# Kernel tuning notes

Hardware: AMD Instinct MI355X
Metric: run time of the kernel (lower is better)

Reference implementation:

```python
import jax, jax.numpy as jnp
import numpy as np

EMB = 512
HEAD = 64
B, S = 4, 4096


def setup_inputs() -> dict:
    key = jax.random.key(0)
    kq, kk, kv, kwq, kwk, kwv = jax.random.split(key, 6)
    q = jax.random.normal(kq, (B, S, EMB), dtype=jnp.float32)
    k = jax.random.normal(kk, (B, S, EMB), dtype=jnp.float32)
    v = jax.random.normal(kv, (B, S, EMB), dtype=jnp.float32)
    # nn.Linear weights: [out_features, in_features], no bias
    sc = 1.0 / np.sqrt(EMB)
    Wq = jax.random.uniform(kwq, (HEAD, EMB), jnp.float32, -sc, sc)
    Wk = jax.random.uniform(kwk, (HEAD, EMB), jnp.float32, -sc, sc)
    Wv = jax.random.uniform(kwv, (HEAD, EMB), jnp.float32, -sc, sc)
    return {"q": q, "k": k, "v": v, "Wq": Wq, "Wk": Wk, "Wv": Wv}


def reference(q, k, v, Wq, Wk, Wv):
    scale = 1.0 / np.sqrt(HEAD).astype(np.float32)
    Q = jnp.einsum('bse,he->bsh', q, Wq)  # [B,S,HEAD]
    K = jnp.einsum('bse,he->bsh', k, Wk)
    V = jnp.einsum('bse,he->bsh', v, Wv)
    scores = jnp.einsum('bqh,bkh->bqk', Q, K) * scale  # [B,S,S]
    attn = jax.nn.softmax(scores, axis=-1)
    # dropout p=0.0 -> identity
    out = jnp.einsum('bqk,bkh->bqh', attn, V)  # [B,S,HEAD]
    return out
```

## Files before the change

### kernel.cpp

```cpp
#include <hip/hip_runtime.h>
#include <hip/hip_bf16.h>

#define EMB    512
#define HEAD   64
#define SEQ    4096
#define NB     4
#define NSPLIT 8
#define LDX    72

#define SL2E   0.18033688011112042f

typedef __bf16 bf16x8 __attribute__((ext_vector_type(8)));
typedef float  f32x4  __attribute__((ext_vector_type(4)));

__device__ inline ushort4 cvt4(float4 v) {
    __hip_bfloat16 a = __float2bfloat16(v.x), b = __float2bfloat16(v.y);
    __hip_bfloat16 c = __float2bfloat16(v.z), d = __float2bfloat16(v.w);
    ushort4 r;
    r.x = *(unsigned short*)&a; r.y = *(unsigned short*)&b;
    r.z = *(unsigned short*)&c; r.w = *(unsigned short*)&d;
    return r;
}

__global__ __launch_bounds__(256) void cvtw_kernel(
    const float* __restrict__ Wq, const float* __restrict__ Wk,
    const float* __restrict__ Wv, __hip_bfloat16* __restrict__ Wc)
{
    int idx   = blockIdx.x * 256 + threadIdx.x;
    int which = idx >> 13;
    int off   = (idx & 8191) * 4;
    const float* src = (which == 0) ? Wq : (which == 1) ? Wk : Wv;
    float s = (which == 0) ? SL2E : 1.0f;
    float4 v = *(const float4*)(src + off);
    v.x *= s; v.y *= s; v.z *= s; v.w *= s;
    *(ushort4*)(Wc + which * 64 * EMB + off) = cvt4(v);
}

__global__ __launch_bounds__(256) void proj_kernel(
    const float* __restrict__ q, const float* __restrict__ k, const float* __restrict__ v,
    const __hip_bfloat16* __restrict__ Wc,
    __hip_bfloat16* __restrict__ Qo, __hip_bfloat16* __restrict__ Ko,
    __hip_bfloat16* __restrict__ Vto)
{
    __shared__ __hip_bfloat16 Xs[32][LDX];

    const int which = blockIdx.y;
    const float* __restrict__ x = (which == 0) ? q : (which == 1) ? k : v;
    const __hip_bfloat16* __restrict__ W = Wc + which * 64 * EMB;

    const int tid  = threadIdx.x;
    const int wave = tid >> 6, lane = tid & 63;
    const int l16  = lane & 15, quad = lane >> 4;
    const int rs   = (wave & 1) * 16;
    const int ch   = wave >> 1;
    const int r0   = blockIdx.x * 32;
    const float* __restrict__ xb = x + (size_t)r0 * EMB;

    const int sr = tid >> 4;
    const int sc = (tid & 15) << 2;

    const f32x4 z = {0.f, 0.f, 0.f, 0.f};
    f32x4 acc[2] = {z, z};

    float4 xr[2];
    bf16x8 wf[4];

#define LOADX(dst, e0)                                                        \
    _Pragma("unroll")                                                         \
    for (int it = 0; it < 2; ++it)                                            \
        dst[it] = *(const float4*)(xb + (size_t)(it * 16 + sr) * EMB + (e0) + sc);

#define LOADW(dst, e0)                                                        \
    _Pragma("unroll")                                                         \
    for (int st = 0; st < 2; ++st)                                            \
        _Pragma("unroll")                                                     \
        for (int tt = 0; tt < 2; ++tt)                                        \
            dst[st * 2 + tt] = *(const bf16x8*)(W + (size_t)((ch * 2 + tt) * 16 + l16) * EMB \
                                                + (e0) + st * 32 + quad * 8);

    LOADX(xr, 0);
    LOADW(wf, 0);

    #pragma unroll
    for (int c = 0; c < 8; ++c) {
        const int e0 = c * 64;
        if (c) __syncthreads();
        #pragma unroll
        for (int it = 0; it < 2; ++it)
            *(ushort4*)&Xs[it * 16 + sr][sc] = cvt4(xr[it]);
        __syncthreads();

        bf16x8 a0 = *(const bf16x8*)&Xs[rs + l16][quad * 8];
        bf16x8 a1 = *(const bf16x8*)&Xs[rs + l16][32 + quad * 8];

        float4 xr2[2];
        bf16x8 wf2[4];
        if (c < 7) { LOADX(xr2, e0 + 64); LOADW(wf2, e0 + 64); }

        #pragma unroll
        for (int tt = 0; tt < 2; ++tt)
            acc[tt] = __builtin_amdgcn_mfma_f32_16x16x32_bf16(a0, wf[tt], acc[tt], 0, 0, 0);
        #pragma unroll
        for (int tt = 0; tt < 2; ++tt)
            acc[tt] = __builtin_amdgcn_mfma_f32_16x16x32_bf16(a1, wf[2 + tt], acc[tt], 0, 0, 0);

        if (c < 7) {
            #pragma unroll
            for (int it = 0; it < 2; ++it) xr[it] = xr2[it];
            #pragma unroll
            for (int j = 0; j < 4; ++j) wf[j] = wf2[j];
        }
    }
#undef LOADX
#undef LOADW

    #pragma unroll
    for (int tt = 0; tt < 2; ++tt) {
        #pragma unroll
        for (int r = 0; r < 4; ++r) {
            int row = r0 + rs + quad * 4 + r;
            int h   = (ch * 2 + tt) * 16 + l16;
            __hip_bfloat16 val = __float2bfloat16(acc[tt][r]);
            if (which == 0) {
                Qo[(size_t)row * HEAD + h] = val;
            } else if (which == 1) {
                Ko[(size_t)row * HEAD + h] = val;
            } else {
                int b = row >> 12, s = row & (SEQ - 1);
                Vto[((size_t)b * HEAD + h) * SEQ + s] = val;
            }
        }
    }
}

__global__ __launch_bounds__(256, 4) void attn_kernel(
    const __hip_bfloat16* __restrict__ Qb, const __hip_bfloat16* __restrict__ Kb,
    const __hip_bfloat16* __restrict__ Vt, float* __restrict__ Op,
    float* __restrict__ lp)
{
    __shared__ __hip_bfloat16 Ps[128][LDX];

    const int tid  = threadIdx.x;
    const int wave = tid >> 6, lane = tid & 63;
    const int l16  = lane & 15, quad = lane >> 4;
    const int b    = blockIdx.y;
    const int q0   = blockIdx.x * 128;
    const int j0b  = blockIdx.z * (SEQ / NSPLIT);

    bf16x8 qf[2][2];
    #pragma unroll
    for (int s = 0; s < 2; ++s) {
        const __hip_bfloat16* qrow =
            Qb + ((size_t)b * SEQ + q0 + wave * 32 + s * 16 + l16) * HEAD + quad * 8;
        qf[s][0] = *(const bf16x8*)(qrow);
        qf[s][1] = *(const bf16x8*)(qrow + 32);
    }

    const __hip_bfloat16* __restrict__ Kfb =
        Kb + ((size_t)b * SEQ + l16) * HEAD + quad * 8;
    const __hip_bfloat16* __restrict__ Vfb =
        Vt + ((size_t)b * HEAD + l16) * SEQ + quad * 8;

    const f32x4 z = {0.f, 0.f, 0.f, 0.f};
    f32x4 oacc[2][4] = {{z, z, z, z}, {z, z, z, z}};
    f32x4 lacc[2] = {z, z};

    const __hip_bfloat16 one_bf = __float2bfloat16(1.0f);
    bf16x8 ones;
    #pragma unroll
    for (int j = 0; j < 8; ++j) ones[j] = *(const __bf16*)&one_bf;

    for (int jt = 0; jt < SEQ / NSPLIT; jt += 64) {
        const int j0 = j0b + jt;

        f32x4 sacc[2][4] = {{z, z, z, z}, {z, z, z, z}};
        #pragma unroll
        for (int st = 0; st < 2; ++st) {
            #pragma unroll
            for (int t = 0; t < 4; ++t) {
                bf16x8 kf = *(const bf16x8*)(Kfb + (size_t)(j0 + t * 16) * HEAD + st * 32);
                #pragma unroll
                for (int s = 0; s < 2; ++s)
                    sacc[s][t] = __builtin_amdgcn_mfma_f32_16x16x32_bf16(kf, qf[s][st], sacc[s][t], 0, 0, 0);
            }
        }

        #pragma unroll
        for (int s = 0; s < 2; ++s)
            #pragma unroll
            for (int t = 0; t < 4; ++t) {
                float4 p;
                p.x = __builtin_amdgcn_exp2f(sacc[s][t][0]);
                p.y = __builtin_amdgcn_exp2f(sacc[s][t][1]);
                p.z = __builtin_amdgcn_exp2f(sacc[s][t][2]);
                p.w = __builtin_amdgcn_exp2f(sacc[s][t][3]);
                *(ushort4*)&Ps[wave * 32 + s * 16 + l16][t * 16 + quad * 4] = cvt4(p);
            }

        #pragma unroll
        for (int st = 0; st < 2; ++st) {
            bf16x8 vf[4];
            #pragma unroll
            for (int t = 0; t < 4; ++t)
                vf[t] = *(const bf16x8*)(Vfb + (size_t)(t * 16) * SEQ + j0 + st * 32);
            #pragma unroll
            for (int s = 0; s < 2; ++s) {
                bf16x8 pf = *(const bf16x8*)&Ps[wave * 32 + s * 16 + l16][st * 32 + quad * 8];
                lacc[s] = __builtin_amdgcn_mfma_f32_16x16x32_bf16(pf, ones, lacc[s], 0, 0, 0);
                #pragma unroll
                for (int t = 0; t < 4; ++t)
                    oacc[s][t] = __builtin_amdgcn_mfma_f32_16x16x32_bf16(pf, vf[t], oacc[s][t], 0, 0, 0);
            }
        }
    }

    const size_t pb = (size_t)(blockIdx.z * NB + b) * SEQ;
    #pragma unroll
    for (int s = 0; s < 2; ++s) {
        const size_t row0 = pb + q0 + wave * 32 + s * 16 + quad * 4;
        if (l16 == 0) {
            #pragma unroll
            for (int r = 0; r < 4; ++r)
                lp[row0 + r] = lacc[s][r];
        }
        #pragma unroll
        for (int t = 0; t < 4; ++t)
            #pragma unroll
            for (int r = 0; r < 4; ++r)
                Op[(row0 + r) * HEAD + t * 16 + l16] = oacc[s][t][r];
    }
}

__global__ __launch_bounds__(256) void merge_kernel(
    const float* __restrict__ Op, const float* __restrict__ lp,
    float* __restrict__ out)
{
    int idx = blockIdx.x * 256 + threadIdx.x;
    int bq  = idx >> 4;
    int c4  = (idx & 15) * 4;
    float4 acc = {0.f, 0.f, 0.f, 0.f};
    float  l   = 0.f;
    #pragma unroll
    for (int s = 0; s < NSPLIT; ++s) {
        float4 o = *(const float4*)(Op + ((size_t)s * NB * SEQ + bq) * HEAD + c4);
        acc.x += o.x; acc.y += o.y; acc.z += o.z; acc.w += o.w;
        l += lp[(size_t)s * NB * SEQ + bq];
    }
    float inv = 1.f / l;
    float4 r = {acc.x * inv, acc.y * inv, acc.z * inv, acc.w * inv};
    *(float4*)(out + (size_t)bq * HEAD + c4) = r;
}

extern "C" void kernel_launch(void* const* d_in, const int* in_sizes, int n_in,
                              void* d_out, int out_size, void* d_ws, size_t ws_size,
                              hipStream_t stream) {
    const float* q  = (const float*)d_in[0];
    const float* k  = (const float*)d_in[1];
    const float* v  = (const float*)d_in[2];
    const float* Wq = (const float*)d_in[3];
    const float* Wk = (const float*)d_in[4];
    const float* Wv = (const float*)d_in[5];
    float* out = (float*)d_out;

    __hip_bfloat16* Qb = (__hip_bfloat16*)d_ws;
    __hip_bfloat16* Kb = Qb + (size_t)NB * SEQ * HEAD;
    __hip_bfloat16* Vt = Kb + (size_t)NB * SEQ * HEAD;
    __hip_bfloat16* Wc = Vt + (size_t)NB * SEQ * HEAD;
    float* Op = (float*)(Wc + 3 * 64 * EMB);
    float* lp = Op + (size_t)NSPLIT * NB * SEQ * HEAD;

    cvtw_kernel<<<96, 256, 0, stream>>>(Wq, Wk, Wv, Wc);

    dim3 pgrid(NB * SEQ / 32, 3);
    proj_kernel<<<pgrid, dim3(256), 0, stream>>>(q, k, v, Wc, Qb, Kb, Vt);

    dim3 agrid(SEQ / 128, NB, NSPLIT);
    attn_kernel<<<agrid, dim3(256), 0, stream>>>(Qb, Kb, Vt, Op, lp);

    merge_kernel<<<(NB * SEQ * 16) / 256, dim3(256), 0, stream>>>(Op, lp, out);
}
```

Measured before the change: 208.4 us.

## Stage K and V tiles through shared memory with register prefetch

The attention kernel no longer has each wave read K and V fragments straight from global memory. The block now loads each 64-key K and V tile cooperatively into LDS and prefetches the next tile into registers while computing on the current one. This removes the four-fold redundant global loads across waves and hides load latency. In exchange it adds two barriers per tile, more LDS per block that may reduce occupancy, and extra registers for the prefetch.

```diff
diff --git a/kernel.cpp b/kernel.cpp
--- a/kernel.cpp
+++ b/kernel.cpp
@@ -138,6 +138,8 @@
     const __hip_bfloat16* __restrict__ Vt, float* __restrict__ Op,
     float* __restrict__ lp)
 {
+    __shared__ __hip_bfloat16 Ks[64][LDX];
+    __shared__ __hip_bfloat16 Vs[64][LDX];
     __shared__ __hip_bfloat16 Ps[128][LDX];
 
     const int tid  = threadIdx.x;
@@ -146,6 +148,7 @@
     const int b    = blockIdx.y;
     const int q0   = blockIdx.x * 128;
     const int j0b  = blockIdx.z * (SEQ / NSPLIT);
+    const int NT   = SEQ / NSPLIT / 64;
 
     bf16x8 qf[2][2];
     #pragma unroll
@@ -156,11 +159,6 @@
         qf[s][1] = *(const bf16x8*)(qrow + 32);
     }
 
-    const __hip_bfloat16* __restrict__ Kfb =
-        Kb + ((size_t)b * SEQ + l16) * HEAD + quad * 8;
-    const __hip_bfloat16* __restrict__ Vfb =
-        Vt + ((size_t)b * HEAD + l16) * SEQ + quad * 8;
-
     const f32x4 z = {0.f, 0.f, 0.f, 0.f};
     f32x4 oacc[2][4] = {{z, z, z, z}, {z, z, z, z}};
     f32x4 lacc[2] = {z, z};
@@ -170,15 +168,38 @@
     #pragma unroll
     for (int j = 0; j < 8; ++j) ones[j] = *(const __bf16*)&one_bf;
 
-    for (int jt = 0; jt < SEQ / NSPLIT; jt += 64) {
-        const int j0 = j0b + jt;
+    const int sr0 = tid >> 3;
+    const int sc8 = (tid & 7) * 8;
+
+#define STAGE_LOAD(j0)                                                        \
+    _Pragma("unroll")                                                         \
+    for (int it = 0; it < 2; ++it) {                                          \
+        int r = sr0 + it * 32;                                                \
+        kr[it] = *(const uint4*)(Kb + ((size_t)b * SEQ + (j0) + r) * HEAD + sc8); \
+        vr[it] = *(const uint4*)(Vt + ((size_t)b * HEAD + r) * SEQ + (j0) + sc8); \
+    }
+
+    uint4 kr[2], vr[2];
+    STAGE_LOAD(j0b);
+
+    for (int jt = 0; jt < NT; ++jt) {
+        __syncthreads();
+        #pragma unroll
+        for (int it = 0; it < 2; ++it) {
+            int r = sr0 + it * 32;
+            *(uint4*)&Ks[r][sc8] = kr[it];
+            *(uint4*)&Vs[r][sc8] = vr[it];
+        }
+        __syncthreads();
+
+        if (jt + 1 < NT) { STAGE_LOAD(j0b + (jt + 1) * 64); }
 
         f32x4 sacc[2][4] = {{z, z, z, z}, {z, z, z, z}};
         #pragma unroll
         for (int st = 0; st < 2; ++st) {
             #pragma unroll
             for (int t = 0; t < 4; ++t) {
-                bf16x8 kf = *(const bf16x8*)(Kfb + (size_t)(j0 + t * 16) * HEAD + st * 32);
+                bf16x8 kf = *(const bf16x8*)&Ks[t * 16 + l16][st * 32 + quad * 8];
                 #pragma unroll
                 for (int s = 0; s < 2; ++s)
                     sacc[s][t] = __builtin_amdgcn_mfma_f32_16x16x32_bf16(kf, qf[s][st], sacc[s][t], 0, 0, 0);
@@ -202,7 +223,7 @@
             bf16x8 vf[4];
             #pragma unroll
             for (int t = 0; t < 4; ++t)
-                vf[t] = *(const bf16x8*)(Vfb + (size_t)(t * 16) * SEQ + j0 + st * 32);
+                vf[t] = *(const bf16x8*)&Vs[t * 16 + l16][st * 32 + quad * 8];
             #pragma unroll
             for (int s = 0; s < 2; ++s) {
                 bf16x8 pf = *(const bf16x8*)&Ps[wave * 32 + s * 16 + l16][st * 32 + quad * 8];
@@ -213,6 +234,7 @@
             }
         }
     }
+#undef STAGE_LOAD
 
     const size_t pb = (size_t)(blockIdx.z * NB + b) * SEQ;
     #pragma unroll
```

Measured after the change: 194.7 us. -6.6%, faster.
